# Optimization experiments

Hardware: AMD Instinct MI355X
Metric: run time of the kernel (lower is better)

## Reference

```python
import jax, jax.numpy as jnp
from jax import lax
import numpy as np

DN = ('NCHW', 'OIHW', 'NCHW')


def _conv(x, w, b):
    y = lax.conv_general_dilated(x, w, (1, 1), 'SAME', dimension_numbers=DN)
    return y + b[None, :, None, None]


def setup_inputs() -> dict:
    key = jax.random.key(0)
    ks = jax.random.split(key, 8)
    B = 2
    noise = 0.1 * jax.random.normal(ks[0], (B, 768, 577), dtype=jnp.float32)  # N(0, 0.1)
    targets = jax.random.randint(ks[1], (B, 384, 384), 0, 171)
    w1 = 0.02 * jax.random.normal(ks[2], (512, 768, 3, 3), dtype=jnp.float32)
    b1 = 0.02 * jax.random.normal(ks[3], (512,), dtype=jnp.float32)
    w2 = 0.02 * jax.random.normal(ks[4], (512, 512, 3, 3), dtype=jnp.float32)
    b2 = 0.02 * jax.random.normal(ks[5], (512,), dtype=jnp.float32)
    w3 = 0.2 * jax.random.normal(ks[6], (77,), dtype=jnp.float32)  # Con3: Conv2d(1,77,1x1)
    b3 = 0.2 * jax.random.normal(ks[7], (77,), dtype=jnp.float32)
    return {'noise': noise, 'targets': targets, 'w1': w1, 'b1': b1,
            'w2': w2, 'b2': b2, 'w3': w3, 'b3': b3}


def reference(noise, targets, w1, b1, w2, b2, w3, b3):
    B = noise.shape[0]
    # NoiseToImage is shadowed by an empty nn.Sequential() -> identity
    image_noise = jnp.transpose(noise, (2, 0, 1))  # (577, B, 768)

    # --- NoiseToText ---
    H, W = targets.shape[1], targets.shape[2]
    ih = (jnp.arange(24) * H) // 24  # nearest-neighbor interpolate indices
    iw = (jnp.arange(24) * W) // 24
    m = targets[:, ih][:, :, iw]  # (B, 24, 24) class labels
    # one-hot scatter into 256 channels, keep first 171 (labels >=171 -> all-zero)
    mask = (m[:, None] == jnp.arange(171)[None, :, None, None]).astype(noise.dtype)  # (B,171,24,24)

    x = noise[:, :, 1:].reshape(B, 768, 24, 24)  # drop CLS token
    xm = x[:, None] * mask[:, :, None]            # (B,171,768,24,24)
    xm = xm.reshape(B * 171, 768, 24, 24)

    y = _conv(xm, w1, b1)                         # (B*171,512,24,24)
    y = y.reshape(-1, 512, 6, 4, 6, 4).mean(axis=(3, 5))  # AdaptiveAvgPool2d((6,6))
    y = _conv(y, w2, b2)                          # (B*171,512,6,6)
    y = y.mean(axis=(2, 3))                       # AdaptiveAvgPool2d((1,1)) -> (B*171,512)
    y = y.reshape(B, 171, 1, 512).transpose(0, 2, 1, 3)  # (B,1,171,512)
    # Con3: 1x1 conv with in_channels=1, out_channels=77
    text_noise = w3[None, :, None, None] * y + b3[None, :, None, None]  # (B,77,171,512)
    return image_noise, text_noise
```

## Files before the change

kernel.cpp:

```cpp
#include <hip/hip_runtime.h>
#include <hip/hip_bf16.h>

typedef unsigned short u16;
typedef short bf16x8 __attribute__((ext_vector_type(8)));
typedef float f32x4 __attribute__((ext_vector_type(4)));

__device__ __forceinline__ u16 f2bf(float f){
    unsigned u = __float_as_uint(f);
    unsigned r = 0x7fffu + ((u >> 16) & 1u);
    return (u16)((u + r) >> 16);
}

__device__ __forceinline__ void gload_lds16(const u16* g, u16* lds_base){
    __builtin_amdgcn_global_load_lds(
        (const __attribute__((address_space(1))) unsigned int*)g,
        (__attribute__((address_space(3))) unsigned int*)lds_base, 16, 0, 0);
}

#define OUT0_N 886272
#define OUT1_N 13483008
#define YN 175104
#define KS2 12

__global__ void k_prep(const float* __restrict__ noise, const int* __restrict__ targets,
                       const float* __restrict__ w1, const float* __restrict__ b1,
                       const float* __restrict__ w2,
                       float* __restrict__ out0, u16* __restrict__ XbfT,
                       u16* __restrict__ Are, u16* __restrict__ Mfull16,
                       float* __restrict__ biasH, int* __restrict__ labels,
                       u16* __restrict__ Zcat16){
    __shared__ float sh[32 * 33];
    int blk = blockIdx.x;
    int tid = threadIdx.x;
    if (blk < 912){
        int b   = blk / 456;
        int rem = blk % 456;
        int cb  = rem / 19, sb = rem % 19;
        int tx = tid & 31, ty = tid >> 5;
        int s0 = sb * 32, c0 = cb * 32;
        float (*tile)[33] = (float(*)[33])sh;
        #pragma unroll
        for (int i = 0; i < 4; i++){
            int c = c0 + ty + i * 8;
            int s = s0 + tx;
            if (s < 577) tile[ty + i * 8][tx] = noise[(size_t)(b * 768 + c) * 577 + s];
        }
        __syncthreads();
        #pragma unroll
        for (int i = 0; i < 4; i++){
            int s = s0 + ty + i * 8;
            int c = c0 + tx;
            if (s >= 577) continue;
            float v = tile[tx][ty + i * 8];
            out0[(size_t)(s * 2 + b) * 768 + c] = v;
            if (s >= 1) XbfT[(size_t)(b * 576 + s - 1) * 768 + c] = f2bf(v);
        }
    } else if (blk < 2448){
        int idx = (blk - 912) * 256 + tid;
        int k = idx % 768; int c1 = idx / 768;
        const float* wp = w1 + (size_t)idx * 9;
        #pragma unroll
        for (int tap = 0; tap < 9; tap++)
            Are[(size_t)(c1 * 9 + tap) * 768 + k] = f2bf(wp[tap]);
    } else if (blk < 3472){
        int b2i = blk - 2448;
        int c2 = b2i >> 1, h = b2i & 1;
        int c1 = h * 256 + tid;
        const float* wp = w2 + (size_t)(c2 * 512 + c1) * 9;
        float t[3][3];
        #pragma unroll
        for (int r = 0; r < 3; r++)
            #pragma unroll
            for (int s = 0; s < 3; s++)
                t[r][s] = wp[r * 3 + s];
        float cs0[3], cs1[3], cs2[3];
        #pragma unroll
        for (int r = 0; r < 3; r++){
            cs0[r] = t[r][0] + t[r][1];
            cs1[r] = t[r][0] + t[r][1] + t[r][2];
            cs2[r] = t[r][1] + t[r][2];
        }
        const float inv = 1.0f / 576.0f;
        u16* Mp = Mfull16 + (size_t)(c2 * 512 + c1) * 9;
        Mp[0] = f2bf(inv * (cs0[0] + cs0[1]));
        Mp[1] = f2bf(inv * (cs1[0] + cs1[1]));
        Mp[2] = f2bf(inv * (cs2[0] + cs2[1]));
        Mp[3] = f2bf(inv * (cs0[0] + cs0[1] + cs0[2]));
        Mp[4] = f2bf(inv * (cs1[0] + cs1[1] + cs1[2]));
        Mp[5] = f2bf(inv * (cs2[0] + cs2[1] + cs2[2]));
        Mp[6] = f2bf(inv * (cs0[1] + cs0[2]));
        Mp[7] = f2bf(inv * (cs1[1] + cs1[2]));
        Mp[8] = f2bf(inv * (cs2[1] + cs2[2]));
        float s_cw = 25.f * (t[0][0] + t[0][2] + t[2][0] + t[2][2])
                   + 30.f * (t[0][1] + t[1][0] + t[1][2] + t[2][1])
                   + 36.f * t[1][1];
        sh[tid] = b1[c1] * s_cw;
        __syncthreads();
        for (int o = 128; o > 0; o >>= 1){ if (tid < o) sh[tid] += sh[tid + o]; __syncthreads(); }
        if (tid == 0) biasH[h * 512 + c2] = sh[0] * (1.0f / 36.0f);
    } else if (blk < 3477){
        int idx = (blk - 3472) * 256 + tid;
        if (idx < 1152){
            int b = idx / 576; int p = idx % 576;
            int i = p / 24, j = p % 24;
            labels[idx] = targets[b * 147456 + i * 16 * 384 + j * 16];
        }
    } else {
        int idx = (blk - 3477) * 256 + tid;
        if (idx < 193536) Zcat16[342 * 4608 + idx] = 0;
    }
}

__launch_bounds__(256)
__global__ void k_gemm1(const u16* __restrict__ Are, const u16* __restrict__ XbfT,
                        float* __restrict__ D){
    __shared__ u16 As[96 * 64];
    __shared__ u16 Bs[128 * 64];
    int tid  = threadIdx.x;
    int wave = tid >> 6, lane = tid & 63;
    int l16 = lane & 15, quad = lane >> 4;
    int wm = wave >> 1, wn = wave & 1;
    int m0 = blockIdx.x * 96;
    int n0 = blockIdx.y * 128;
    int srow = lane >> 3, scol = (lane & 7) * 8;
    f32x4 acc[3][4] = {};
    for (int k0 = 0; k0 < 768; k0 += 64){
        #pragma unroll
        for (int j = 0; j < 3; j++){
            int ch = wave * 3 + j;
            gload_lds16(Are + (size_t)(m0 + ch * 8 + srow) * 768 + k0 + scol, &As[ch * 512]);
        }
        #pragma unroll
        for (int j = 0; j < 4; j++){
            int ch = wave * 4 + j;
            gload_lds16(XbfT + (size_t)(n0 + ch * 8 + srow) * 768 + k0 + scol, &Bs[ch * 512]);
        }
        __syncthreads();
        #pragma unroll
        for (int ks = 0; ks < 2; ks++){
            bf16x8 af[3], bf[4];
            #pragma unroll
            for (int i = 0; i < 3; i++)
                af[i] = *(const bf16x8*)&As[(wm * 48 + i * 16 + l16) * 64 + ks * 32 + quad * 8];
            #pragma unroll
            for (int i = 0; i < 4; i++)
                bf[i] = *(const bf16x8*)&Bs[(wn * 64 + i * 16 + l16) * 64 + ks * 32 + quad * 8];
            #pragma unroll
            for (int mi = 0; mi < 3; mi++)
                #pragma unroll
                for (int ni = 0; ni < 4; ni++)
                    acc[mi][ni] = __builtin_amdgcn_mfma_f32_16x16x32_bf16(af[mi], bf[ni], acc[mi][ni], 0, 0, 0);
        }
        __syncthreads();
    }
    #pragma unroll
    for (int mi = 0; mi < 3; mi++)
        #pragma unroll
        for (int ni = 0; ni < 4; ni++)
            #pragma unroll
            for (int r = 0; r < 4; r++)
                D[(size_t)(m0 + wm * 48 + mi * 16 + quad * 4 + r) * 1152 + n0 + wn * 64 + ni * 16 + l16] = acc[mi][ni][r];
}

__launch_bounds__(256)
__global__ void k_scatter(const float* __restrict__ D, const int* __restrict__ labels,
                          u16* __restrict__ Zcat16){
    int blk = blockIdx.x;
    int b  = blk >> 9;
    int c1 = blk & 511;
    __shared__ float acc[171 * 9];
    int t = threadIdx.x;
    for (int q = t; q < 1539; q += 256) acc[q] = 0.f;
    __syncthreads();
    for (int p = t; p < 576; p += 256){
        int cls = labels[b * 576 + p];
        if (cls < 0 || cls >= 171) continue;
        int i = p / 24, j = p % 24;
        float slot[9];
        #pragma unroll
        for (int q = 0; q < 9; q++) slot[q] = 0.f;
        unsigned used = 0;
        int tau[3]; bool vs[3];
        #pragma unroll
        for (int s1 = 0; s1 < 3; s1++){
            int v = j - s1 + 1;
            vs[s1]  = (v >= 0 && v < 24);
            tau[s1] = (v < 4) ? 0 : ((v < 20) ? 1 : 2);
        }
        #pragma unroll
        for (int r1 = 0; r1 < 3; r1++){
            int u = i - r1 + 1;
            if (u < 0 || u >= 24) continue;
            int rho = (u < 4) ? 0 : ((u < 20) ? 1 : 2);
            #pragma unroll
            for (int s1 = 0; s1 < 3; s1++){
                if (!vs[s1]) continue;
                float tv = D[(size_t)(c1 * 9 + r1 * 3 + s1) * 1152 + b * 576 + p];
                int sl = rho * 3 + tau[s1];
                slot[sl] += tv;
                used |= 1u << sl;
            }
        }
        #pragma unroll
        for (int sl = 0; sl < 9; sl++)
            if (used & (1u << sl)) atomicAdd(&acc[cls * 9 + sl], slot[sl]);
    }
    __syncthreads();
    for (int q = t; q < 1539; q += 256){
        int cls = q / 9, sl = q % 9;
        Zcat16[(size_t)(b * 171 + cls) * 4608 + c1 * 9 + sl] = f2bf(acc[q]);
    }
}

__launch_bounds__(256)
__global__ void k_gemm2m(const u16* __restrict__ Zcat16, const u16* __restrict__ Mfull16,
                         float* __restrict__ ypart){
    __shared__ u16 As[128 * 64];
    __shared__ u16 Bs[64 * 64];
    int tid  = threadIdx.x;
    int wave = tid >> 6, lane = tid & 63;
    int l16 = lane & 15, quad = lane >> 4;
    int wm = wave >> 1, wn = wave & 1;
    int m0 = blockIdx.x * 128;
    int n0 = blockIdx.y * 64;
    int kbeg = blockIdx.z * 384;
    int srow = lane >> 3, scol = (lane & 7) * 8;
    f32x4 acc[4][2] = {};
    for (int k0 = kbeg; k0 < kbeg + 384; k0 += 64){
        #pragma unroll
        for (int j = 0; j < 4; j++){
            int ch = wave * 4 + j;
            gload_lds16(Zcat16 + (size_t)(m0 + ch * 8 + srow) * 4608 + k0 + scol, &As[ch * 512]);
        }
        #pragma unroll
        for (int j = 0; j < 2; j++){
            int ch = wave * 2 + j;
            gload_lds16(Mfull16 + (size_t)(n0 + ch * 8 + srow) * 4608 + k0 + scol, &Bs[ch * 512]);
        }
        __syncthreads();
        #pragma unroll
        for (int ks = 0; ks < 2; ks++){
            bf16x8 af[4], bf[2];
            #pragma unroll
            for (int i = 0; i < 4; i++)
                af[i] = *(const bf16x8*)&As[(wm * 64 + i * 16 + l16) * 64 + ks * 32 + quad * 8];
            #pragma unroll
            for (int i = 0; i < 2; i++)
                bf[i] = *(const bf16x8*)&Bs[(wn * 32 + i * 16 + l16) * 64 + ks * 32 + quad * 8];
            #pragma unroll
            for (int mi = 0; mi < 4; mi++)
                #pragma unroll
                for (int ni = 0; ni < 2; ni++)
                    acc[mi][ni] = __builtin_amdgcn_mfma_f32_16x16x32_bf16(af[mi], bf[ni], acc[mi][ni], 0, 0, 0);
        }
        __syncthreads();
    }
    float* yp = ypart + (size_t)blockIdx.z * YN;
    #pragma unroll
    for (int mi = 0; mi < 4; mi++)
        #pragma unroll
        for (int r = 0; r < 4; r++){
            int n = m0 + wm * 64 + mi * 16 + quad * 4 + r;
            if (n >= 342) continue;
            #pragma unroll
            for (int ni = 0; ni < 2; ni++)
                yp[(size_t)n * 512 + n0 + wn * 32 + ni * 16 + l16] = acc[mi][ni][r];
        }
}

__global__ void k_red(const float* __restrict__ ypart, const float* __restrict__ biasH,
                      const float* __restrict__ b2, float4* __restrict__ ysum){
    int idx = blockIdx.x * 128 + threadIdx.x;
    int c4 = idx & 127;
    int n  = idx >> 7;
    float4 sum = ((const float4*)b2)[c4];
    float4 ba  = ((const float4*)biasH)[c4];
    float4 bb  = ((const float4*)biasH)[128 + c4];
    sum.x += ba.x + bb.x; sum.y += ba.y + bb.y; sum.z += ba.z + bb.z; sum.w += ba.w + bb.w;
    #pragma unroll
    for (int s = 0; s < KS2; s++){
        float4 v = *(const float4*)&ypart[(size_t)s * YN + (size_t)n * 512 + c4 * 4];
        sum.x += v.x; sum.y += v.y; sum.z += v.z; sum.w += v.w;
    }
    ysum[idx] = sum;
}

__global__ void k_expand(const float4* __restrict__ ysum, const float* __restrict__ w3,
                         const float* __restrict__ b3, float4* __restrict__ out1){
    int idx = blockIdx.x * 256 + threadIdx.x;
    if (idx >= OUT1_N / 4) return;
    int c4 = idx & 127;
    int t  = idx >> 7;
    int cls = t % 171;
    int u   = t / 171;
    int o   = u % 77;
    int b   = u / 77;
    float w  = w3[o];
    float bb = b3[o];
    float4 v = ysum[(b * 171 + cls) * 128 + c4];
    out1[idx] = make_float4(w * v.x + bb, w * v.y + bb, w * v.z + bb, w * v.w + bb);
}

extern "C" void kernel_launch(void* const* d_in, const int* in_sizes, int n_in,
                              void* d_out, int out_size, void* d_ws, size_t ws_size,
                              hipStream_t stream) {
    const float* noise   = (const float*)d_in[0];
    const int*   targets = (const int*)  d_in[1];
    const float* w1      = (const float*)d_in[2];
    const float* b1      = (const float*)d_in[3];
    const float* w2      = (const float*)d_in[4];
    const float* b2      = (const float*)d_in[5];
    const float* w3      = (const float*)d_in[6];
    const float* b3      = (const float*)d_in[7];
    float* out0 = (float*)d_out;
    float* out1 = out0 + OUT0_N;

    char* ws = (char*)d_ws;
    const size_t OFF_ARE  = 0;
    const size_t OFF_X    = 7077888;
    const size_t OFF_D    = OFF_X   + 1769472;
    const size_t OFF_MF   = OFF_D   + 21233664;
    const size_t OFF_ZC   = OFF_MF  + 4718592;
    const size_t OFF_BH   = OFF_ZC  + 3538944;
    const size_t OFF_LAB  = OFF_BH  + 4096;
    const size_t OFF_YS   = OFF_LAB + 4608;

    u16*   Are    = (u16*)  (ws + OFF_ARE);
    u16*   XbfT   = (u16*)  (ws + OFF_X);
    float* D      = (float*)(ws + OFF_D);
    float* ypart  = (float*)(ws + OFF_D);
    u16*   Mfull16= (u16*)  (ws + OFF_MF);
    u16*   Zcat16 = (u16*)  (ws + OFF_ZC);
    float* biasH  = (float*)(ws + OFF_BH);
    int*   labels = (int*)  (ws + OFF_LAB);
    float* ysum   = (float*)(ws + OFF_YS);

    k_prep  <<<4233, 256, 0, stream>>>(noise, targets, w1, b1, w2,
                                       out0, XbfT, Are, Mfull16, biasH, labels, Zcat16);
    k_gemm1 <<<dim3(48, 9), 256, 0, stream>>>(Are, XbfT, D);
    k_scatter<<<1024, 256, 0, stream>>>(D, labels, Zcat16);
    k_gemm2m<<<dim3(3, 8, KS2), 256, 0, stream>>>(Zcat16, Mfull16, ypart);
    k_red   <<<342, 128, 0, stream>>>(ypart, biasH, b2, (float4*)ysum);
    k_expand<<<13167, 256, 0, stream>>>((const float4*)ysum, w3, b3, (float4*)out1);
}
```

Before: 156.8 us.

## Double-buffer gemm1 LDS tiles with XOR swizzle and larger M tile

Restructures the first GEMM kernel to use double-buffered LDS stages, so the async global-to-LDS loads for the next K slice overlap MFMA compute on the current one, with explicit vmcnt waits and raw barriers. It also XOR-swizzles LDS columns to reduce bank conflicts and doubles the M tile to 192 rows per block, halving the grid. This trades more LDS and accumulator registers and fewer blocks (216) for better latency hiding and data reuse.

```diff
diff --git a/kernel.cpp b/kernel.cpp
--- a/kernel.cpp
+++ b/kernel.cpp
@@ -15,6 +15,12 @@
     __builtin_amdgcn_global_load_lds(
         (const __attribute__((address_space(1))) unsigned int*)g,
         (__attribute__((address_space(3))) unsigned int*)lds_base, 16, 0, 0);
+}
+
+__device__ __forceinline__ void wgbar(){
+    asm volatile("" ::: "memory");
+    __builtin_amdgcn_s_barrier();
+    asm volatile("" ::: "memory");
 }
 
 #define OUT0_N 886272
@@ -114,52 +120,82 @@
 __launch_bounds__(256)
 __global__ void k_gemm1(const u16* __restrict__ Are, const u16* __restrict__ XbfT,
                         float* __restrict__ D){
-    __shared__ u16 As[96 * 64];
-    __shared__ u16 Bs[128 * 64];
+    __shared__ u16 As[2][192 * 64];
+    __shared__ u16 Bs[2][128 * 64];
     int tid  = threadIdx.x;
     int wave = tid >> 6, lane = tid & 63;
     int l16 = lane & 15, quad = lane >> 4;
     int wm = wave >> 1, wn = wave & 1;
-    int m0 = blockIdx.x * 96;
+    int m0 = blockIdx.x * 192;
     int n0 = blockIdx.y * 128;
-    int srow = lane >> 3, scol = (lane & 7) * 8;
-    f32x4 acc[3][4] = {};
-    for (int k0 = 0; k0 < 768; k0 += 64){
-        #pragma unroll
-        for (int j = 0; j < 3; j++){
-            int ch = wave * 3 + j;
-            gload_lds16(Are + (size_t)(m0 + ch * 8 + srow) * 768 + k0 + scol, &As[ch * 512]);
+    int srow = lane >> 3;
+    int scol = ((lane & 7) * 8) ^ (srow * 8);
+    int rx   = (l16 & 7) * 8;
+    const u16* Ag = Are  + (size_t)(m0 + srow) * 768 + scol;
+    const u16* Bg = XbfT + (size_t)(n0 + srow) * 768 + scol;
+    f32x4 acc[6][4] = {};
+
+    auto stage = [&](int buf, int k0){
+        #pragma unroll
+        for (int j = 0; j < 6; j++){
+            int ch = wave * 6 + j;
+            gload_lds16(Ag + (size_t)ch * 8 * 768 + k0, &As[buf][ch * 512]);
         }
         #pragma unroll
         for (int j = 0; j < 4; j++){
             int ch = wave * 4 + j;
-            gload_lds16(XbfT + (size_t)(n0 + ch * 8 + srow) * 768 + k0 + scol, &Bs[ch * 512]);
-        }
-        __syncthreads();
+            gload_lds16(Bg + (size_t)ch * 8 * 768 + k0, &Bs[buf][ch * 512]);
+        }
+    };
+    auto compute = [&](int buf){
         #pragma unroll
         for (int ks = 0; ks < 2; ks++){
-            bf16x8 af[3], bf[4];
-            #pragma unroll
-            for (int i = 0; i < 3; i++)
-                af[i] = *(const bf16x8*)&As[(wm * 48 + i * 16 + l16) * 64 + ks * 32 + quad * 8];
+            int kc = (ks * 32 + quad * 8) ^ rx;
+            bf16x8 af[6], bf[4];
+            #pragma unroll
+            for (int i = 0; i < 6; i++)
+                af[i] = *(const bf16x8*)&As[buf][(wm * 96 + i * 16 + l16) * 64 + kc];
             #pragma unroll
             for (int i = 0; i < 4; i++)
-                bf[i] = *(const bf16x8*)&Bs[(wn * 64 + i * 16 + l16) * 64 + ks * 32 + quad * 8];
-            #pragma unroll
-            for (int mi = 0; mi < 3; mi++)
+                bf[i] = *(const bf16x8*)&Bs[buf][(wn * 64 + i * 16 + l16) * 64 + kc];
+            #pragma unroll
+            for (int mi = 0; mi < 6; mi++)
                 #pragma unroll
                 for (int ni = 0; ni < 4; ni++)
                     acc[mi][ni] = __builtin_amdgcn_mfma_f32_16x16x32_bf16(af[mi], bf[ni], acc[mi][ni], 0, 0, 0);
         }
-        __syncthreads();
-    }
+    };
+
+    stage(0, 0);
+    #pragma unroll 1
+    for (int t = 0; t < 10; t += 2){
+        stage(1, (t + 1) * 64);
+        asm volatile("s_waitcnt vmcnt(10)" ::: "memory");
+        wgbar();
+        compute(0);
+        wgbar();
+        stage(0, (t + 2) * 64);
+        asm volatile("s_waitcnt vmcnt(10)" ::: "memory");
+        wgbar();
+        compute(1);
+        wgbar();
+    }
+    stage(1, 11 * 64);
+    asm volatile("s_waitcnt vmcnt(10)" ::: "memory");
+    wgbar();
+    compute(0);
+    wgbar();
+    asm volatile("s_waitcnt vmcnt(0)" ::: "memory");
+    wgbar();
+    compute(1);
+
     #pragma unroll
-    for (int mi = 0; mi < 3; mi++)
+    for (int mi = 0; mi < 6; mi++)
         #pragma unroll
         for (int ni = 0; ni < 4; ni++)
             #pragma unroll
             for (int r = 0; r < 4; r++)
-                D[(size_t)(m0 + wm * 48 + mi * 16 + quad * 4 + r) * 1152 + n0 + wn * 64 + ni * 16 + l16] = acc[mi][ni][r];
+                D[(size_t)(m0 + wm * 96 + mi * 16 + quad * 4 + r) * 1152 + n0 + wn * 64 + ni * 16 + l16] = acc[mi][ni][r];
 }
 
 __launch_bounds__(256)
@@ -337,7 +373,7 @@
 
     k_prep  <<<4233, 256, 0, stream>>>(noise, targets, w1, b1, w2,
                                        out0, XbfT, Are, Mfull16, biasH, labels, Zcat16);
-    k_gemm1 <<<dim3(48, 9), 256, 0, stream>>>(Are, XbfT, D);
+    k_gemm1 <<<dim3(24, 9), 256, 0, stream>>>(Are, XbfT, D);
     k_scatter<<<1024, 256, 0, stream>>>(D, labels, Zcat16);
     k_gemm2m<<<dim3(3, 8, KS2), 256, 0, stream>>>(Zcat16, Mfull16, ypart);
     k_red   <<<342, 128, 0, stream>>>(ypart, biasH, b2, (float4*)ysum);
```

Result: no change. 156.2 us (-0.4%).
